# Performance work log

Measured on AMD Instinct MI355X. Metric: run time of the kernel, lower is better.

## Reference

```python
import jax, jax.numpy as jnp
import numpy as np

NEG_INF = -1e9  # finite to keep softmax grads clean


def apply_rope(x, cos, sin):
    # x: [b, s, h, hd]; cos/sin: [s, hd//2] -> interleaved complex rotation (LLaMA style)
    b, s, h, hd = x.shape
    xr = x.reshape(b, s, h, hd // 2, 2)
    x_re, x_im = xr[..., 0], xr[..., 1]
    c = cos[None, :, None, :]
    sn = sin[None, :, None, :]
    o_re = x_re * c - x_im * sn
    o_im = x_re * sn + x_im * c
    return jnp.stack([o_re, o_im], axis=-1).reshape(b, s, h, hd)


def setup_inputs() -> dict:
    key = jax.random.key(0)
    ks = jax.random.split(key, 8)
    bs, seq, d = 2, 2048, 4096
    n_heads, n_kv, hd = 32, 8, 128
    max_seq = 4096
    x = jax.random.normal(ks[0], (bs, seq, d), jnp.float32)
    sc = 1.0 / np.sqrt(d)
    wq = jax.random.normal(ks[1], (n_heads * hd, d), jnp.float32) * sc
    wk = jax.random.normal(ks[2], (n_kv * hd, d), jnp.float32) * sc
    wv = jax.random.normal(ks[3], (n_kv * hd, d), jnp.float32) * sc
    wo = jax.random.normal(ks[4], (d, n_heads * hd), jnp.float32) * sc
    cache_k = jnp.zeros((bs, max_seq, n_kv, hd), jnp.float32)
    cache_v = jnp.zeros((bs, max_seq, n_kv, hd), jnp.float32)
    # LLaMA rope frequencies
    theta = 500000.0
    inv_freq = 1.0 / (theta ** (np.arange(0, hd, 2, dtype=np.float32) / hd))  # [hd/2]
    t = np.arange(seq, dtype=np.float32)
    ang = np.outer(t, inv_freq)  # [seq, hd/2]
    freqs_rope = jnp.stack([jnp.cos(jnp.asarray(ang)), jnp.sin(jnp.asarray(ang))], axis=0)  # [2, seq, hd/2]
    # causal additive mask [seq, seq]
    mask = jnp.where(jnp.tril(jnp.ones((seq, seq), bool)), 0.0, NEG_INF).astype(jnp.float32)
    return {"x": x, "wq": wq, "wk": wk, "wv": wv, "wo": wo,
            "cache_k": cache_k, "cache_v": cache_v,
            "freqs_rope": freqs_rope, "mask": mask, "start_pos": 0}


def reference(x, wq, wk, wv, wo, cache_k, cache_v, freqs_rope, mask, start_pos):
    bs, seq, d = x.shape
    n_heads, n_kv, hd = 32, 8, 128
    n_rep = n_heads // n_kv

    xq = (x @ wq.T).reshape(bs, seq, n_heads, hd)
    xk = (x @ wk.T).reshape(bs, seq, n_kv, hd)
    xv = (x @ wv.T).reshape(bs, seq, n_kv, hd)

    cos, sin = freqs_rope[0], freqs_rope[1]
    xq = apply_rope(xq, cos, sin)
    xk = apply_rope(xk, cos, sin)

    # KV-cache write (functional), then read [:, :start_pos+seq]
    cache_k = jax.lax.dynamic_update_slice(cache_k, xk, (0, start_pos, 0, 0))
    cache_v = jax.lax.dynamic_update_slice(cache_v, xv, (0, start_pos, 0, 0))
    kv_len = start_pos + seq
    keys = cache_k[:, :kv_len]      # [bs, kv_len, n_kv, hd]
    values = cache_v[:, :kv_len]

    # GQA repeat_kv: [bs, kv_len, n_kv, hd] -> [bs, kv_len, n_kv*n_rep, hd]
    keys = jnp.repeat(keys, n_rep, axis=2)
    values = jnp.repeat(values, n_rep, axis=2)

    q = xq.transpose(0, 2, 1, 3)      # [bs, H, seq, hd]
    k = keys.transpose(0, 2, 1, 3)    # [bs, H, kv_len, hd]
    v = values.transpose(0, 2, 1, 3)

    scores = jnp.einsum("bhqd,bhkd->bhqk", q, k) * (hd ** -0.5)
    scores = scores + mask
    attn = jax.nn.softmax(scores, axis=-1)
    out = jnp.einsum("bhqk,bhkd->bhqd", attn, v)
    out = out.transpose(0, 2, 1, 3).reshape(bs, seq, n_heads * hd)
    return out @ wo.T
```

## Files before the change

kernel.cpp:

```cpp
#include <hip/hip_runtime.h>

typedef __bf16 bf16x8 __attribute__((ext_vector_type(8)));
typedef short short8_t __attribute__((ext_vector_type(8)));
typedef float f32x4 __attribute__((ext_vector_type(4)));
typedef float f32x16 __attribute__((ext_vector_type(16)));
typedef int int2v __attribute__((ext_vector_type(2)));
typedef unsigned short us4_t __attribute__((ext_vector_type(4)));

#define SCALE 0.08838834764831845f
#define CEXP 0.1275179f

#define VMCNT(n) asm volatile("s_waitcnt vmcnt(" #n ")" ::: "memory")

__device__ __forceinline__ float b2f(unsigned short u) {
  union { unsigned int i; float f; } v; v.i = ((unsigned int)u) << 16; return v.f;
}
__device__ __forceinline__ unsigned short f2b(float f) {
  union { float f; unsigned int i; } v; v.f = f;
  unsigned int r = v.i + 0x7fffu + ((v.i >> 16) & 1u);
  return (unsigned short)(r >> 16);
}
__device__ __forceinline__ int packtr(float lo, float hi_) {
  unsigned a = __builtin_bit_cast(unsigned, lo) >> 16;
  unsigned b = __builtin_bit_cast(unsigned, hi_) & 0xffff0000u;
  return (int)(a | b);
}

__device__ __forceinline__ f32x4 mfma16(short8_t a, short8_t b, f32x4 c) {
  return __builtin_amdgcn_mfma_f32_16x16x32_bf16(
      __builtin_bit_cast(bf16x8, a), __builtin_bit_cast(bf16x8, b), c, 0, 0, 0);
}
__device__ __forceinline__ f32x16 mfma32(short8_t a, short8_t b, f32x16 c) {
  return __builtin_amdgcn_mfma_f32_32x32x16_bf16(
      __builtin_bit_cast(bf16x8, a), __builtin_bit_cast(bf16x8, b), c, 0, 0, 0);
}

typedef __attribute__((address_space(1))) const void gas_t;
typedef __attribute__((address_space(3))) void las_t;
__device__ __forceinline__ void gload16(const void* g, void* l) {
  __builtin_amdgcn_global_load_lds((gas_t*)g, (las_t*)l, 16, 0, 0);
}

__global__ void cvt_kernel(const float* __restrict__ src, unsigned short* __restrict__ dst, int n4) {
  for (int i = blockIdx.x * blockDim.x + threadIdx.x; i < n4; i += gridDim.x * blockDim.x) {
    f32x4 v = *(const f32x4*)(src + (size_t)i * 4);
    us4_t o;
    o[0] = f2b(v[0]); o[1] = f2b(v[1]); o[2] = f2b(v[2]); o[3] = f2b(v[3]);
    *(us4_t*)(dst + (size_t)i * 4) = o;
  }
}

template <int MODE>
__device__ __forceinline__ void gemm256_core(
    unsigned short* __restrict__ lds,
    const unsigned short* __restrict__ A, const unsigned short* __restrict__ Bt,
    void* __restrict__ Cout, int m0, int n0, int K, int ldc) {
  const int tid = threadIdx.x;
  const int wid = tid >> 6, lane = tid & 63;
  const int ln = lane & 15, lg = lane >> 4;
  const int wm = wid >> 2, wn = wid & 3;
  const int NT = K >> 5;

  const int sr0 = wid * 16 + (lane >> 2);
  const int sr1 = 128 + sr0;
  const int sj0 = ((lane & 3) ^ ((sr0 >> 1) & 3)) * 8;
  const int sj1 = ((lane & 3) ^ ((sr1 >> 1) & 3)) * 8;
  const unsigned short* gA0 = A + (size_t)(m0 + sr0) * K + sj0;
  const unsigned short* gA1 = A + (size_t)(m0 + sr1) * K + sj1;
  const unsigned short* gB0 = Bt + (size_t)(n0 + sr0) * K + sj0;
  const unsigned short* gB1 = Bt + (size_t)(n0 + sr1) * K + sj1;
  unsigned short* dA = lds + wid * 512;
  unsigned short* dB = lds + 32768 + wid * 512;

  const int swz = (ln >> 1) & 3;
  const int jA = (lg ^ swz) << 4;
  const unsigned char* ldsb = (const unsigned char*)lds;
  const int aoff = (wm * 128 + ln) * 64 + jA;
  const int boff = 65536 + (wn * 64 + ln) * 64 + jA;

  f32x4 acc[8][4] = {};

#define STAGE_A(t_) { int s_ = (t_) & 3; int k0_ = (t_) << 5; \
    gload16(gA0 + k0_, dA + s_ * 8192); \
    gload16(gA1 + k0_, dA + s_ * 8192 + 4096); }
#define STAGE_B(t_) { int s_ = (t_) & 3; int k0_ = (t_) << 5; \
    gload16(gB0 + k0_, dB + s_ * 8192); \
    gload16(gB1 + k0_, dB + s_ * 8192 + 4096); }

  STAGE_A(0); STAGE_B(0);
  STAGE_A(1); STAGE_B(1);
  STAGE_A(2); STAGE_B(2);
  VMCNT(8);
  __builtin_amdgcn_s_barrier();

  for (int t = 0; t < NT; ++t) {
    const int sb = (t & 3) * 16384;
    if (t + 3 < NT) { STAGE_A(t + 3); STAGE_B(t + 3); }
    short8_t af[8], bf[4];
#pragma unroll
    for (int mi = 0; mi < 8; ++mi)
      af[mi] = *(const short8_t*)(ldsb + sb + aoff + mi * 1024);
#pragma unroll
    for (int nj = 0; nj < 4; ++nj)
      bf[nj] = *(const short8_t*)(ldsb + sb + boff + nj * 1024);
    if (t < NT - 3) { VMCNT(8); }
    else if (t == NT - 3) { VMCNT(4); }
    else if (t == NT - 2) { VMCNT(0); }
    __builtin_amdgcn_s_barrier();
    asm volatile("s_waitcnt lgkmcnt(0)" ::: "memory");
    __builtin_amdgcn_sched_barrier(0);
    __builtin_amdgcn_s_setprio(1);
#pragma unroll
    for (int mi = 0; mi < 8; ++mi)
#pragma unroll
      for (int nj = 0; nj < 4; ++nj)
        acc[mi][nj] = mfma16(af[mi], bf[nj], acc[mi][nj]);
    __builtin_amdgcn_s_setprio(0);
    __builtin_amdgcn_s_barrier();
  }
#undef STAGE_A
#undef STAGE_B

#pragma unroll
  for (int mi = 0; mi < 8; ++mi) {
#pragma unroll
    for (int nj = 0; nj < 4; ++nj) {
#pragma unroll
      for (int r = 0; r < 4; ++r) {
        int row = m0 + wm * 128 + mi * 16 + lg * 4 + r;
        int col = n0 + wn * 64 + nj * 16 + ln;
        if (MODE == 1)
          ((unsigned short*)Cout)[(size_t)row * ldc + col] = f2b(acc[mi][nj][r]);
        else
          ((float*)Cout)[(size_t)row * ldc + col] = acc[mi][nj][r];
      }
    }
  }
}

template <int MODE>
__device__ __forceinline__ void gemm128(unsigned short* __restrict__ ldsbuf,
                                        const unsigned short* __restrict__ A,
                                        const unsigned short* __restrict__ Bt,
                                        void* __restrict__ Cout,
                                        int m0, int n0, int K, int ldc) {
  unsigned short* As = ldsbuf;
  unsigned short* Bs = ldsbuf + 4096;
  const int tid = threadIdx.x;
  const int wave = tid >> 6, lane = tid & 63;
  const int ln = lane & 15, g = lane >> 4;
  const int wm = (wave >> 1) * 64, wn = (wave & 1) * 64;

  const int rA0 = wave * 16 + (lane >> 2);
  const int rA1 = 64 + wave * 16 + (lane >> 2);
  const int colx = (lane & 3) * 8;
  const unsigned short* gA0 = A + (size_t)(m0 + rA0) * K + colx;
  const unsigned short* gA1 = A + (size_t)(m0 + rA1) * K + colx;
  const unsigned short* gB0 = Bt + (size_t)(n0 + rA0) * K + colx;
  const unsigned short* gB1 = Bt + (size_t)(n0 + rA1) * K + colx;
  unsigned short* lA0 = As + wave * 512;
  unsigned short* lA1 = As + 2048 + wave * 512;
  unsigned short* lB0 = Bs + wave * 512;
  unsigned short* lB1 = Bs + 2048 + wave * 512;

  f32x4 acc[4][4] = {};

  for (int k0 = 0; k0 < K; k0 += 32) {
    gload16(gA0 + k0, lA0);
    gload16(gA1 + k0, lA1);
    gload16(gB0 + k0, lB0);
    gload16(gB1 + k0, lB1);
    __syncthreads();
    short8_t a[4], b[4];
#pragma unroll
    for (int i = 0; i < 4; ++i)
      a[i] = *(const short8_t*)(As + (wm + i * 16 + ln) * 32 + g * 8);
#pragma unroll
    for (int j = 0; j < 4; ++j)
      b[j] = *(const short8_t*)(Bs + (wn + j * 16 + ln) * 32 + g * 8);
#pragma unroll
    for (int i = 0; i < 4; ++i)
#pragma unroll
      for (int j = 0; j < 4; ++j)
        acc[i][j] = mfma16(a[i], b[j], acc[i][j]);
    __syncthreads();
  }

#pragma unroll
  for (int i = 0; i < 4; ++i) {
#pragma unroll
    for (int j = 0; j < 4; ++j) {
      if (MODE == 2) {
        int row0 = m0 + wm + i * 16 + g * 4;
        int col = n0 + wn + j * 16 + ln;
        us4_t pk;
#pragma unroll
        for (int r = 0; r < 4; ++r) pk[r] = f2b(acc[i][j][r]);
        *(us4_t*)((unsigned short*)Cout +
                  ((size_t)((row0 >> 11) * 1024 + col)) * 2048 + (row0 & 2047)) = pk;
      } else {
#pragma unroll
        for (int r = 0; r < 4; ++r) {
          int row = m0 + wm + i * 16 + g * 4 + r;
          int col = n0 + wn + j * 16 + ln;
          ((unsigned short*)Cout)[(size_t)row * ldc + col] = f2b(acc[i][j][r]);
        }
      }
    }
  }
}

__global__ __launch_bounds__(512, 1) void gemm_q_kernel(
    const unsigned short* __restrict__ xb, const unsigned short* __restrict__ wqb,
    unsigned short* __restrict__ xq) {
  __shared__ __align__(16) unsigned short lds[65536];
  gemm256_core<1>(lds, xb, wqb, xq, blockIdx.y * 256, blockIdx.x * 256, 4096, 4096);
}

__global__ __launch_bounds__(256) void gemm_kv_kernel(
    const unsigned short* __restrict__ xb, const unsigned short* __restrict__ wkb,
    const unsigned short* __restrict__ wvb, unsigned short* __restrict__ xk,
    unsigned short* __restrict__ xvT) {
  __shared__ __align__(16) unsigned short lds[8192];
  int bx = blockIdx.x, by = blockIdx.y;
  if (bx < 8) gemm128<1>(lds, xb, wkb, xk, by * 128, bx * 128, 4096, 1024);
  else        gemm128<2>(lds, xb, wvb, xvT, by * 128, (bx - 8) * 128, 4096, 0);
}

__global__ __launch_bounds__(512, 1) void gemm_o_kernel(
    const unsigned short* __restrict__ ao, const unsigned short* __restrict__ wob,
    float* __restrict__ out) {
  __shared__ __align__(16) unsigned short lds[65536];
  gemm256_core<0>(lds, ao, wob, out, blockIdx.y * 256, blockIdx.x * 256, 4096, 4096);
}

template <int NH>
__global__ void rope_kernel(unsigned short* __restrict__ p, const float* __restrict__ fr,
                            int nchunks) {
  for (int c = blockIdx.x * blockDim.x + threadIdx.x; c < nchunks;
       c += gridDim.x * blockDim.x) {
    size_t e = (size_t)c * 8;
    int f0 = (c & 15) * 4;
    int rest = (int)(e >> 7);
    int s = (rest / NH) & 2047;
    unsigned short* ptr = p + e;
    short8_t v = *(short8_t*)ptr;
    const float* cosp = fr + (size_t)s * 64 + f0;
    const float* sinp = cosp + 131072;
#pragma unroll
    for (int j = 0; j < 4; ++j) {
      float re = b2f((unsigned short)v[2 * j]);
      float im = b2f((unsigned short)v[2 * j + 1]);
      float cc = cosp[j], ss = sinp[j];
      v[2 * j]     = (short)f2b(re * cc - im * ss);
      v[2 * j + 1] = (short)f2b(re * ss + im * cc);
    }
    *(short8_t*)ptr = v;
  }
}

__global__ __launch_bounds__(512, 2) void attn_kernel(
    const unsigned short* __restrict__ xq, const unsigned short* __restrict__ xk,
    const unsigned short* __restrict__ xvT, unsigned short* __restrict__ ao) {
  __shared__ __align__(16) unsigned char smem[56320];
  const int tid = threadIdx.x;
  const int wq = tid >> 6, lane = tid & 63;
  const int q31 = lane & 31, hi = lane >> 5;
  const int bx = blockIdx.z ? (int)blockIdx.x : 7 - (int)blockIdx.x;
  const int h = blockIdx.y, b = blockIdx.z;
  const int hkv = h >> 2;
  const int q0 = bx * 256;
  const int a0 = q0 + wq * 32;
  const int ktmax_w = a0 >> 6;
  const int NT = bx * 4 + 4;

  const unsigned short* kbase = xk + ((size_t)(b * 2048) * 8 + hkv) * 128;
  const unsigned short* vtg = xvT + (size_t)(b * 1024 + hkv * 128) * 2048;

  const unsigned short* qrow = xq + ((size_t)(b * 2048 + a0 + q31) * 32 + h) * 128;
  short8_t qf[8];
#pragma unroll
  for (int st = 0; st < 8; ++st) qf[st] = *(const short8_t*)(qrow + st * 16 + hi * 8);

  const int c0 = tid, c1 = tid + 512;
  const int kg0 = (c0 >> 4) * 1024 + (c0 & 15) * 8;
  const int kg1 = (c1 >> 4) * 1024 + (c1 & 15) * 8;
  const int ka0 = (c0 >> 4) * 256 + (((c0 & 15) ^ ((c0 >> 4) & 7)) << 4);
  const int ka1 = (c1 >> 4) * 256 + (((c1 & 15) ^ ((c1 >> 4) & 7)) << 4);
  const int d0 = tid >> 3, kb0 = tid & 7, d1v = d0 + 64;
  const int vg0 = d0 * 2048 + kb0 * 8, vg1 = d1v * 2048 + kb0 * 8;
  const int va0 = d0 * 72 + kb0 * 8, va1 = d1v * 72 + kb0 * 8;

  unsigned short* Kb = (unsigned short*)(smem);
  unsigned short* VT = (unsigned short*)(smem + 16384);
  unsigned short* pp = (unsigned short*)(smem + 34816) + wq * 1280;
  unsigned short* prow = pp + q31 * 40;
  float* cl = (float*)(smem + 55296) + wq * 32;

  f32x16 o[4] = {};
  float m_run = -1e30f, l_run = 0.f;

  short8_t kr0 = *(const short8_t*)(kbase + kg0);
  short8_t kr1 = *(const short8_t*)(kbase + kg1);
  short8_t vr0 = *(const short8_t*)(vtg + vg0);
  short8_t vr1 = *(const short8_t*)(vtg + vg1);

  for (int kt = 0; kt < NT; ++kt) {
    *(short8_t*)((unsigned char*)Kb + ka0) = kr0;
    *(short8_t*)((unsigned char*)Kb + ka1) = kr1;
    *(short8_t*)(VT + va0) = vr0;
    *(short8_t*)(VT + va1) = vr1;
    __syncthreads();
    if (kt + 1 < NT) {
      const unsigned short* kg = kbase + (size_t)(kt + 1) * 65536;
      kr0 = *(const short8_t*)(kg + kg0);
      kr1 = *(const short8_t*)(kg + kg1);
      vr0 = *(const short8_t*)(vtg + vg0 + (kt + 1) * 64);
      vr1 = *(const short8_t*)(vtg + vg1 + (kt + 1) * 64);
    }

    if (kt <= ktmax_w) {
      const int r7 = (q31 & 7) << 4;
      f32x16 p0 = {}, p1 = {};
      __builtin_amdgcn_s_setprio(1);
#pragma unroll
      for (int st = 0; st < 8; ++st) {
        int cb = (((st * 2 + hi) << 4)) ^ r7;
        short8_t k0 = *(const short8_t*)((const unsigned char*)Kb + q31 * 256 + cb);
        short8_t k1 = *(const short8_t*)((const unsigned char*)Kb + (q31 + 32) * 256 + cb);
        p0 = mfma32(k0, qf[st], p0);
        p1 = mfma32(k1, qf[st], p1);
      }
      __builtin_amdgcn_s_setprio(0);

      if (kt == ktmax_w) {
        const int q = a0 + q31;
#pragma unroll
        for (int r = 0; r < 16; ++r) {
          int crow = (r & 3) + 8 * (r >> 2) + 4 * hi;
          int kgl = kt * 64 + crow;
          if (kgl > q) p0[r] = -1e30f;
          if (kgl + 32 > q) p1[r] = -1e30f;
        }
      }
      float mx = -1e30f;
#pragma unroll
      for (int r = 0; r < 16; ++r) mx = fmaxf(mx, fmaxf(p0[r], p1[r]));
      mx = fmaxf(mx, __shfl_xor(mx, 32));
      const bool defer = __all(mx <= m_run + 30.0f);
      const float mnew = defer ? m_run : fmaxf(m_run, mx);
      float sum = 0.f;
#pragma unroll
      for (int r = 0; r < 16; ++r) {
        p0[r] = exp2f((p0[r] - mnew) * CEXP);
        p1[r] = exp2f((p1[r] - mnew) * CEXP);
        sum += p0[r] + p1[r];
      }
      sum += __shfl_xor(sum, 32);
      if (defer) {
        l_run += sum;
      } else {
        float corr = exp2f((m_run - mnew) * CEXP);
        m_run = mnew;
        l_run = l_run * corr + sum;
        cl[q31] = corr;
        f32x4 cv0 = *(const f32x4*)(cl + hi * 4);
        f32x4 cv1 = *(const f32x4*)(cl + 8 + hi * 4);
        f32x4 cv2 = *(const f32x4*)(cl + 16 + hi * 4);
        f32x4 cv3 = *(const f32x4*)(cl + 24 + hi * 4);
#pragma unroll
        for (int db = 0; db < 4; ++db) {
#pragma unroll
          for (int r = 0; r < 4; ++r) {
            o[db][r]      *= cv0[r];
            o[db][4 + r]  *= cv1[r];
            o[db][8 + r]  *= cv2[r];
            o[db][12 + r] *= cv3[r];
          }
        }
      }

#pragma unroll
      for (int u = 0; u < 4; ++u) {
        int2v w;
        w[0] = packtr(p0[4 * u], p0[4 * u + 1]);
        w[1] = packtr(p0[4 * u + 2], p0[4 * u + 3]);
        *(int2v*)(prow + u * 8 + hi * 4) = w;
      }
      {
        short8_t pa0 = *(const short8_t*)(prow + hi * 8);
        short8_t pa1 = *(const short8_t*)(prow + 16 + hi * 8);
        __builtin_amdgcn_s_setprio(1);
#pragma unroll
        for (int db = 0; db < 4; ++db) {
          const unsigned short* vtd = VT + (db * 32 + q31) * 72;
          short8_t vf0 = *(const short8_t*)(vtd + hi * 8);
          short8_t vf1 = *(const short8_t*)(vtd + 16 + hi * 8);
          o[db] = mfma32(pa0, vf0, o[db]);
          o[db] = mfma32(pa1, vf1, o[db]);
        }
        __builtin_amdgcn_s_setprio(0);
      }
#pragma unroll
      for (int u = 0; u < 4; ++u) {
        int2v w;
        w[0] = packtr(p1[4 * u], p1[4 * u + 1]);
        w[1] = packtr(p1[4 * u + 2], p1[4 * u + 3]);
        *(int2v*)(prow + u * 8 + hi * 4) = w;
      }
      {
        short8_t pa2 = *(const short8_t*)(prow + hi * 8);
        short8_t pa3 = *(const short8_t*)(prow + 16 + hi * 8);
        __builtin_amdgcn_s_setprio(1);
#pragma unroll
        for (int db = 0; db < 4; ++db) {
          const unsigned short* vtd = VT + (db * 32 + q31) * 72;
          short8_t vf2 = *(const short8_t*)(vtd + 32 + hi * 8);
          short8_t vf3 = *(const short8_t*)(vtd + 48 + hi * 8);
          o[db] = mfma32(pa2, vf2, o[db]);
          o[db] = mfma32(pa3, vf3, o[db]);
        }
        __builtin_amdgcn_s_setprio(0);
      }
    }
    __syncthreads();
  }

  cl[q31] = l_run;
  f32x4 lv0 = *(const f32x4*)(cl + hi * 4);
  f32x4 lv1 = *(const f32x4*)(cl + 8 + hi * 4);
  f32x4 lv2 = *(const f32x4*)(cl + 16 + hi * 4);
  f32x4 lv3 = *(const f32x4*)(cl + 24 + hi * 4);
  f32x4 iv0, iv1, iv2, iv3;
#pragma unroll
  for (int r = 0; r < 4; ++r) {
    iv0[r] = 1.0f / lv0[r]; iv1[r] = 1.0f / lv1[r];
    iv2[r] = 1.0f / lv2[r]; iv3[r] = 1.0f / lv3[r];
  }
  unsigned short* ob = ao + ((size_t)(b * 2048 + a0) * 32 + h) * 128;
#pragma unroll
  for (int db = 0; db < 4; ++db) {
#pragma unroll
    for (int r = 0; r < 16; ++r) {
      int crow = (r & 3) + 8 * (r >> 2) + 4 * hi;
      float iv = (r < 4) ? iv0[r & 3] : (r < 8) ? iv1[r & 3] : (r < 12) ? iv2[r & 3] : iv3[r & 3];
      ob[(size_t)crow * 4096 + db * 32 + q31] = f2b(o[db][r] * iv);
    }
  }
}

extern "C" void kernel_launch(void* const* d_in, const int* in_sizes, int n_in,
                              void* d_out, int out_size, void* d_ws, size_t ws_size,
                              hipStream_t stream) {
  const float* x  = (const float*)d_in[0];
  const float* wq = (const float*)d_in[1];
  const float* wk = (const float*)d_in[2];
  const float* wv = (const float*)d_in[3];
  const float* wo = (const float*)d_in[4];
  const float* fr = (const float*)d_in[7];
  float* out = (float*)d_out;

  char* ws = (char*)d_ws;
  unsigned short* xb  = (unsigned short*)(ws);
  unsigned short* wqb = (unsigned short*)(ws + 33554432);
  unsigned short* wkb = (unsigned short*)(ws + 67108864);
  unsigned short* wvb = (unsigned short*)(ws + 75497472);
  unsigned short* xq  = (unsigned short*)(ws + 83886080);
  unsigned short* xk  = (unsigned short*)(ws + 117440512);
  unsigned short* xvT = (unsigned short*)(ws + 125829120);
  unsigned short* ao  = xb;
  unsigned short* wob = wqb;

  dim3 blk(256);
  cvt_kernel<<<dim3(1024), blk, 0, stream>>>(x,  xb,  16777216 / 4);
  cvt_kernel<<<dim3(1024), blk, 0, stream>>>(wq, wqb, 16777216 / 4);
  cvt_kernel<<<dim3(512),  blk, 0, stream>>>(wk, wkb, 4194304 / 4);
  cvt_kernel<<<dim3(512),  blk, 0, stream>>>(wv, wvb, 4194304 / 4);

  gemm_q_kernel<<<dim3(16, 16), dim3(512), 0, stream>>>(xb, wqb, xq);
  gemm_kv_kernel<<<dim3(16, 32), dim3(256), 0, stream>>>(xb, wkb, wvb, xk, xvT);

  rope_kernel<32><<<dim3(2048), blk, 0, stream>>>(xq, fr, 2097152);
  rope_kernel<8><<<dim3(512),  blk, 0, stream>>>(xk, fr, 524288);

  cvt_kernel<<<dim3(1024), blk, 0, stream>>>(wo, wob, 16777216 / 4);

  attn_kernel<<<dim3(8, 32, 2), dim3(512), 0, stream>>>(xq, xk, xvT, ao);

  gemm_o_kernel<<<dim3(16, 16), dim3(512), 0, stream>>>(ao, wob, out);
}
```

Measured before the change: 531.2 us.

## Restructure GEMM main loop to K=64 double-buffered tiles with split-phase staging

The 256x256 GEMM core now uses 64-wide K tiles with two LDS buffers instead of 32-wide tiles with four buffers. Each iteration is split into four phases that interleave the next tile's staged loads (A-low, A-high, B-low, B-high) with MFMA blocks. The LDS swizzle changes to an 8-chunk XOR pattern to suit the wider rows. The aim is to halve loop and barrier overhead per K element and to spread global loads across compute phases. The cost is more barriers per iteration and a shallower prefetch distance, which may expose memory latency.

```diff
diff --git a/kernel.cpp b/kernel.cpp
--- a/kernel.cpp
+++ b/kernel.cpp
@@ -59,67 +59,112 @@
   const int wid = tid >> 6, lane = tid & 63;
   const int ln = lane & 15, lg = lane >> 4;
   const int wm = wid >> 2, wn = wid & 3;
-  const int NT = K >> 5;
-
-  const int sr0 = wid * 16 + (lane >> 2);
-  const int sr1 = 128 + sr0;
-  const int sj0 = ((lane & 3) ^ ((sr0 >> 1) & 3)) * 8;
-  const int sj1 = ((lane & 3) ^ ((sr1 >> 1) & 3)) * 8;
-  const unsigned short* gA0 = A + (size_t)(m0 + sr0) * K + sj0;
-  const unsigned short* gA1 = A + (size_t)(m0 + sr1) * K + sj1;
-  const unsigned short* gB0 = Bt + (size_t)(n0 + sr0) * K + sj0;
-  const unsigned short* gB1 = Bt + (size_t)(n0 + sr1) * K + sj1;
-  unsigned short* dA = lds + wid * 512;
-  unsigned short* dB = lds + 32768 + wid * 512;
-
-  const int swz = (ln >> 1) & 3;
-  const int jA = (lg ^ swz) << 4;
+  const int NT = K >> 6;
+
+  const int c0 = tid, c1 = tid + 512;
+  const int r0 = c0 >> 3, r1 = c1 >> 3;
+  const int sb0 = (((c0 & 7) ^ ((r0 >> 1) & 7)) << 3);
+  const int sb1 = (((c1 & 7) ^ ((r1 >> 1) & 7)) << 3);
+  const unsigned short* gA0 = A + (size_t)(m0 + r0) * K + sb0;
+  const unsigned short* gA1 = A + (size_t)(m0 + r1) * K + sb1;
+  const unsigned short* gB0 = Bt + (size_t)(n0 + r0) * K + sb0;
+  const unsigned short* gB1 = Bt + (size_t)(n0 + r1) * K + sb1;
+  const size_t rowK128 = (size_t)128 * K;
+  unsigned short* d0 = lds + c0 * 8;
+  unsigned short* d1 = lds + c1 * 8;
+
+  const int s3 = (ln >> 1) & 7;
   const unsigned char* ldsb = (const unsigned char*)lds;
-  const int aoff = (wm * 128 + ln) * 64 + jA;
-  const int boff = 65536 + (wn * 64 + ln) * 64 + jA;
+  const int abase = wm * 16384 + ln * 128;
+  const int bbase = 32768 + (wn >> 1) * 16384 + ((wn & 1) * 64 + ln) * 128;
+  const int jt0 = ((lg) ^ s3) << 4;
+  const int jt1 = ((4 + lg) ^ s3) << 4;
 
   f32x4 acc[8][4] = {};
-
-#define STAGE_A(t_) { int s_ = (t_) & 3; int k0_ = (t_) << 5; \
-    gload16(gA0 + k0_, dA + s_ * 8192); \
-    gload16(gA1 + k0_, dA + s_ * 8192 + 4096); }
-#define STAGE_B(t_) { int s_ = (t_) & 3; int k0_ = (t_) << 5; \
-    gload16(gB0 + k0_, dB + s_ * 8192); \
-    gload16(gB1 + k0_, dB + s_ * 8192 + 4096); }
-
-  STAGE_A(0); STAGE_B(0);
-  STAGE_A(1); STAGE_B(1);
-  STAGE_A(2); STAGE_B(2);
-  VMCNT(8);
-  __builtin_amdgcn_s_barrier();
+  short8_t afL[4], afH[4], bf[4];
+
+#define STG(h_, t_) { \
+    const unsigned short* s0_; const unsigned short* s1_; \
+    if ((h_) == 0) { s0_ = gA0; s1_ = gA1; } \
+    else if ((h_) == 1) { s0_ = gA0 + rowK128; s1_ = gA1 + rowK128; } \
+    else if ((h_) == 2) { s0_ = gB0; s1_ = gB1; } \
+    else { s0_ = gB0 + rowK128; s1_ = gB1 + rowK128; } \
+    unsigned short* dd = lds + ((t_) & 1) * 32768 + (h_) * 8192; \
+    gload16(s0_ + (size_t)(t_) * 64, dd + (c0 - tid) * 0 + c0 * 8 - c0 * 8 + c0 * 8); \
+    gload16(s1_ + (size_t)(t_) * 64, dd + c1 * 8); }
+
+  STG(0, 0) STG(1, 0) STG(2, 0) STG(3, 0)
 
   for (int t = 0; t < NT; ++t) {
-    const int sb = (t & 3) * 16384;
-    if (t + 3 < NT) { STAGE_A(t + 3); STAGE_B(t + 3); }
-    short8_t af[8], bf[4];
-#pragma unroll
-    for (int mi = 0; mi < 8; ++mi)
-      af[mi] = *(const short8_t*)(ldsb + sb + aoff + mi * 1024);
-#pragma unroll
-    for (int nj = 0; nj < 4; ++nj)
-      bf[nj] = *(const short8_t*)(ldsb + sb + boff + nj * 1024);
-    if (t < NT - 3) { VMCNT(8); }
-    else if (t == NT - 3) { VMCNT(4); }
-    else if (t == NT - 2) { VMCNT(0); }
-    __builtin_amdgcn_s_barrier();
+    const unsigned char* cb = ldsb + (t & 1) * 65536;
+    if (t + 1 < NT) { STG(0, t + 1) VMCNT(2); } else { VMCNT(0); }
+    __builtin_amdgcn_s_barrier();
+#pragma unroll
+    for (int i = 0; i < 4; ++i)
+      afL[i] = *(const short8_t*)(cb + abase + i * 2048 + jt0);
+#pragma unroll
+    for (int j = 0; j < 4; ++j)
+      bf[j] = *(const short8_t*)(cb + bbase + j * 2048 + jt0);
     asm volatile("s_waitcnt lgkmcnt(0)" ::: "memory");
     __builtin_amdgcn_sched_barrier(0);
     __builtin_amdgcn_s_setprio(1);
 #pragma unroll
-    for (int mi = 0; mi < 8; ++mi)
-#pragma unroll
-      for (int nj = 0; nj < 4; ++nj)
-        acc[mi][nj] = mfma16(af[mi], bf[nj], acc[mi][nj]);
+    for (int i = 0; i < 4; ++i)
+#pragma unroll
+      for (int j = 0; j < 4; ++j)
+        acc[i][j] = mfma16(afL[i], bf[j], acc[i][j]);
     __builtin_amdgcn_s_setprio(0);
     __builtin_amdgcn_s_barrier();
-  }
-#undef STAGE_A
-#undef STAGE_B
+    if (t + 1 < NT) STG(1, t + 1)
+#pragma unroll
+    for (int i = 0; i < 4; ++i)
+      afH[i] = *(const short8_t*)(cb + abase + 8192 + i * 2048 + jt0);
+    __builtin_amdgcn_s_barrier();
+    asm volatile("s_waitcnt lgkmcnt(0)" ::: "memory");
+    __builtin_amdgcn_sched_barrier(0);
+    __builtin_amdgcn_s_setprio(1);
+#pragma unroll
+    for (int i = 0; i < 4; ++i)
+#pragma unroll
+      for (int j = 0; j < 4; ++j)
+        acc[4 + i][j] = mfma16(afH[i], bf[j], acc[4 + i][j]);
+    __builtin_amdgcn_s_setprio(0);
+    __builtin_amdgcn_s_barrier();
+    if (t + 1 < NT) STG(2, t + 1)
+#pragma unroll
+    for (int i = 0; i < 4; ++i)
+      afL[i] = *(const short8_t*)(cb + abase + i * 2048 + jt1);
+#pragma unroll
+    for (int j = 0; j < 4; ++j)
+      bf[j] = *(const short8_t*)(cb + bbase + j * 2048 + jt1);
+    __builtin_amdgcn_s_barrier();
+    asm volatile("s_waitcnt lgkmcnt(0)" ::: "memory");
+    __builtin_amdgcn_sched_barrier(0);
+    __builtin_amdgcn_s_setprio(1);
+#pragma unroll
+    for (int i = 0; i < 4; ++i)
+#pragma unroll
+      for (int j = 0; j < 4; ++j)
+        acc[i][j] = mfma16(afL[i], bf[j], acc[i][j]);
+    __builtin_amdgcn_s_setprio(0);
+    __builtin_amdgcn_s_barrier();
+    if (t + 1 < NT) STG(3, t + 1)
+#pragma unroll
+    for (int i = 0; i < 4; ++i)
+      afH[i] = *(const short8_t*)(cb + abase + 8192 + i * 2048 + jt1);
+    __builtin_amdgcn_s_barrier();
+    asm volatile("s_waitcnt lgkmcnt(0)" ::: "memory");
+    __builtin_amdgcn_sched_barrier(0);
+    __builtin_amdgcn_s_setprio(1);
+#pragma unroll
+    for (int i = 0; i < 4; ++i)
+#pragma unroll
+      for (int j = 0; j < 4; ++j)
+        acc[4 + i][j] = mfma16(afH[i], bf[j], acc[4 + i][j]);
+    __builtin_amdgcn_s_setprio(0);
+    __builtin_amdgcn_s_barrier();
+  }
+#undef STG
 
 #pragma unroll
   for (int mi = 0; mi < 8; ++mi) {
```

After: 506.0 us. -4.7%, faster.
